# Performance work log

Measured on AMD Instinct MI355X. Metric: run time of the kernel, lower is better.

## Reference

```python
import jax, jax.numpy as jnp
import numpy as np

B = 16
C = 80
LEVELS = [(128, 128, 8), (64, 64, 16), (32, 32, 32), (16, 16, 64), (8, 8, 128)]
TOPN = 1000
MIN_SCORE = 0.05
NMS_THR = 0.6
MAX_OBJ = 100


def setup_inputs() -> dict:
    key = jax.random.key(0)
    inp = {}
    for l, (H, W, s) in enumerate(LEVELS):
        key, k1, k2, k3 = jax.random.split(key, 4)
        inp[f"cls{l}"] = jax.random.uniform(k1, (B, H, W, C), jnp.float32)
        inp[f"reg{l}"] = jax.random.uniform(k2, (B, H, W, 4), jnp.float32) * 128.0
        inp[f"ctr{l}"] = jax.random.uniform(k3, (B, H, W, 1), jnp.float32)
        xs = (jnp.arange(W, dtype=jnp.float32) + 0.5) * s
        ys = (jnp.arange(H, dtype=jnp.float32) + 0.5) * s
        gx, gy = jnp.meshgrid(xs, ys)  # [H, W]
        pos = jnp.stack([gx, gy], axis=-1)  # [H, W, 2]
        inp[f"pos{l}"] = jnp.broadcast_to(pos, (B, H, W, 2))
    return inp


def _nms_one(scores, classes, bboxes):
    # scores [N], classes int32 [N], bboxes float [N, 4] (already int-truncated values)
    s = jnp.where(scores > MIN_SCORE, scores, -jnp.inf)  # score-threshold mask
    top_s, top_i = jax.lax.top_k(s, TOPN)  # sort descending, keep topn
    top_c = jax.lax.stop_gradient(classes[top_i].astype(jnp.float32))
    top_b = bboxes[top_i]
    valid = top_s > MIN_SCORE
    wh = top_b[:, 2:4] - top_b[:, 0:2]
    areas = jnp.clip(wh[:, 0] * wh[:, 1], 0.0001)
    ar = jnp.arange(TOPN)

    def body(i, suppressed):
        active = valid[i] & (~suppressed[i])
        b = top_b[i]
        tl = jnp.maximum(b[0:2], top_b[:, 0:2])
        br = jnp.minimum(b[2:4], top_b[:, 2:4])
        owh = jnp.clip(br - tl, 0.0)
        inter = owh[:, 0] * owh[:, 1]
        union = jnp.clip(areas[i] + areas - inter, 0.0001)
        iou = inter / union
        return suppressed | (active & (ar > i) & (iou >= NMS_THR))

    suppressed = jax.lax.fori_loop(0, TOPN, body, jnp.zeros((TOPN,), bool))
    keep = valid & (~suppressed)
    rank = jnp.cumsum(keep.astype(jnp.int32)) - 1
    # scatter kept detections (in score order) into first MAX_OBJ slots; slot MAX_OBJ is a dump
    idx = jnp.where(keep & (rank < MAX_OBJ), rank, MAX_OBJ)
    out_s = jnp.full((MAX_OBJ + 1,), -1.0, jnp.float32).at[idx].set(jnp.where(keep, top_s, -1.0))[:MAX_OBJ]
    out_c = jnp.full((MAX_OBJ + 1,), -1.0, jnp.float32).at[idx].set(jnp.where(keep, top_c, -1.0))[:MAX_OBJ]
    out_b = jnp.zeros((MAX_OBJ + 1, 4), jnp.float32).at[idx].set(jnp.where(keep[:, None], top_b, 0.0))[:MAX_OBJ]
    return out_s, out_c, out_b


def _forward(cls_list, reg_list, ctr_list, pos_list):
    ss, cc, bb = [], [], []
    for c, r, t, p in zip(cls_list, reg_list, ctr_list, pos_list):
        b = c.shape[0]
        c = c.reshape(b, -1, c.shape[-1])   # [B, HW, 80]
        r = r.reshape(b, -1, 4)             # [B, HW, 4]
        t = t.reshape(b, -1)                # [B, HW]
        p = p.reshape(b, -1, 2)             # [B, HW, 2]
        sc = jnp.sqrt(jnp.max(c, axis=2) * t)
        cl = jnp.argmax(c, axis=2).astype(jnp.int32)
        bmin = p - r[:, :, 0:2]
        bmax = p + r[:, :, 2:4]
        # torch .int() truncates toward zero; values are used as floats afterward
        box = jax.lax.stop_gradient(jnp.trunc(jnp.concatenate([bmin, bmax], axis=2)))
        ss.append(sc); cc.append(cl); bb.append(box)
    scores = jnp.concatenate(ss, axis=1)
    classes = jnp.concatenate(cc, axis=1)
    boxes = jnp.concatenate(bb, axis=1)
    return jax.vmap(_nms_one)(scores, classes, boxes)


def reference(cls0, cls1, cls2, cls3, cls4, reg0, reg1, reg2, reg3, reg4,
              ctr0, ctr1, ctr2, ctr3, ctr4, pos0, pos1, pos2, pos3, pos4):
    return _forward([cls0, cls1, cls2, cls3, cls4],
                    [reg0, reg1, reg2, reg3, reg4],
                    [ctr0, ctr1, ctr2, ctr3, ctr4],
                    [pos0, pos1, pos2, pos3, pos4])
```

## Files before the change

### kernel.cpp

```cpp
#include <hip/hip_runtime.h>
#include <stdint.h>

typedef unsigned int u32;
typedef unsigned long long u64;

#define NTOT 21824
#define NBATCH 16
#define TOPN 1000
#define MAXOBJ 100
#define CAP 2048
#define CAPC 8192

__global__ void zero_kernel(u32* __restrict__ h) {
    int i = blockIdx.x * 1024 + threadIdx.x;
    if (i < NBATCH * 2048 + NBATCH * 32) h[i] = 0;
}

__global__ __launch_bounds__(256) void decode_kernel(
    const float* __restrict__ cls0, const float* __restrict__ cls1,
    const float* __restrict__ cls2, const float* __restrict__ cls3,
    const float* __restrict__ cls4,
    const float* __restrict__ ctr0, const float* __restrict__ ctr1,
    const float* __restrict__ ctr2, const float* __restrict__ ctr3,
    const float* __restrict__ ctr4,
    u32* __restrict__ keys, int* __restrict__ clsidx,
    u32* __restrict__ hist0)
{
    __shared__ u32 bh[2048];
    for (int i = threadIdx.x; i < 2048; i += 256) bh[i] = 0;
    __syncthreads();

    int tid = threadIdx.x;
    int g = tid >> 2, j = tid & 3;
    int loc = blockIdx.x * 64 + g;
    int b = blockIdx.y;
    if (loc < NTOT) {
        const float *cp, *tp;
        if (loc < 16384)      { size_t o = (size_t)b*16384 + loc;          cp = cls0 + o*80; tp = ctr0 + o; }
        else if (loc < 20480) { size_t o = (size_t)b*4096  + (loc-16384);  cp = cls1 + o*80; tp = ctr1 + o; }
        else if (loc < 21504) { size_t o = (size_t)b*1024  + (loc-20480);  cp = cls2 + o*80; tp = ctr2 + o; }
        else if (loc < 21760) { size_t o = (size_t)b*256   + (loc-21504);  cp = cls3 + o*80; tp = ctr3 + o; }
        else                  { size_t o = (size_t)b*64    + (loc-21760);  cp = cls4 + o*80; tp = ctr4 + o; }

        const float4* c4 = (const float4*)cp;
        float maxv = -1.0f; int arg = 0;
#pragma unroll
        for (int q = 0; q < 5; ++q) {
            float4 v = c4[j + 4*q];
            int ch = 16*q + 4*j;
            if (v.x > maxv) { maxv = v.x; arg = ch;     }
            if (v.y > maxv) { maxv = v.y; arg = ch + 1; }
            if (v.z > maxv) { maxv = v.z; arg = ch + 2; }
            if (v.w > maxv) { maxv = v.w; arg = ch + 3; }
        }
#pragma unroll
        for (int d = 1; d <= 2; d <<= 1) {
            float ov = __shfl_xor(maxv, d);
            int   oa = __shfl_xor(arg, d);
            if (ov > maxv || (ov == maxv && oa < arg)) { maxv = ov; arg = oa; }
        }
        if (j == 0) {
            float score = sqrtf(maxv * (*tp));
            u32 key = (score > 0.05f) ? (__float_as_uint(score) | 0x80000000u) : 0u;
            size_t o = (size_t)b * NTOT + loc;
            keys[o] = key;
            clsidx[o] = arg;
            if (key) atomicAdd(&bh[key >> 21], 1u);
        }
    }
    __syncthreads();
    for (int i = threadIdx.x; i < 2048; i += 256) {
        u32 c = bh[i];
        if (c) atomicAdd(&hist0[b * 2048 + i], c);
    }
}

__global__ __launch_bounds__(1024) void pivot_kernel(
    const u32* __restrict__ keys, const u32* __restrict__ hist0,
    u32* __restrict__ params,
    float* __restrict__ tscore, float* __restrict__ tcls, float4* __restrict__ tbox)
{
    __shared__ u32 shist[2048];
    __shared__ u32 s_wtot[16];
    __shared__ int s_tf;
    __shared__ u32 s_C, s_above;
    int b = blockIdx.x, tid = threadIdx.x;
    int lane = tid & 63, wave = tid >> 6;
    const u32* kb = keys + (size_t)b * NTOT;

    for (int i = tid; i < TOPN; i += 1024) {
        size_t o = (size_t)b * TOPN + i;
        tscore[o] = -1.0f; tcls[o] = -1.0f;
        tbox[o] = make_float4(0.f, 0.f, 0.f, 0.f);
    }

    u32 h0 = hist0[b * 2048 + 2 * tid];
    u32 h1 = hist0[b * 2048 + 2 * tid + 1];
    if (tid == 0) s_tf = -1;
    u32 x = h0 + h1;
#pragma unroll
    for (int off = 1; off < 64; off <<= 1) {
        u32 y = __shfl_down(x, off);
        if (lane + off < 64) x += y;
    }
    if (lane == 0) s_wtot[wave] = x;
    __syncthreads();
    u32 wsuf = 0, tot = 0;
    for (int w2 = 0; w2 < 16; ++w2) { u32 v = s_wtot[w2]; tot += v; if (w2 > wave) wsuf += v; }
    u32 suf0 = x + wsuf, suf1 = suf0 - h0;
    u32 target = (tot < TOPN) ? tot : TOPN;

    if (target > 0) {
        if (suf0 >= target) atomicMax(&s_tf, 2 * tid);
        if (suf1 >= target) atomicMax(&s_tf, 2 * tid + 1);
    }
    __syncthreads();
    int t0 = s_tf;
    if (target > 0) {
        if (2 * tid == t0)     { s_C = suf0; s_above = suf0 - h0; }
        if (2 * tid + 1 == t0) { s_C = suf1; s_above = suf1 - h1; }
    }
    __syncthreads();
    u32 C0 = (target > 0) ? s_C : 0;
    u32 above0 = (target > 0) ? s_above : 0;

    bool need2 = (target > 0 && C0 > CAP);
    int t1 = 0; u32 C1 = 0, above1 = 0;
    shist[2 * tid] = 0; shist[2 * tid + 1] = 0;
    if (tid == 0) s_tf = -1;
    __syncthreads();
    if (need2) {
        for (int i = tid; i < NTOT; i += 1024) {
            u32 k = kb[i];
            if (k && (int)(k >> 21) == t0) atomicAdd(&shist[(k >> 10) & 2047], 1u);
        }
    }
    __syncthreads();
    {
        u32 g0 = shist[2 * tid], g1 = shist[2 * tid + 1];
        u32 x2 = g0 + g1;
#pragma unroll
        for (int off = 1; off < 64; off <<= 1) {
            u32 y = __shfl_down(x2, off);
            if (lane + off < 64) x2 += y;
        }
        if (lane == 0) s_wtot[wave] = x2;
        __syncthreads();
        u32 ws2 = 0;
        for (int w2 = wave + 1; w2 < 16; ++w2) ws2 += s_wtot[w2];
        u32 sa0 = x2 + ws2, sa1 = sa0 - g0;
        u32 need2c = target - above0;
        if (need2) {
            if (sa0 >= need2c) atomicMax(&s_tf, 2 * tid);
            if (sa1 >= need2c) atomicMax(&s_tf, 2 * tid + 1);
        }
        __syncthreads();
        t1 = s_tf;
        if (need2) {
            if (2 * tid == t1)     { s_C = above0 + sa0; s_above = above0 + sa0 - g0; }
            if (2 * tid + 1 == t1) { s_C = above0 + sa1; s_above = above0 + sa1 - g1; }
        }
        __syncthreads();
        if (need2) { C1 = s_C; above1 = s_above; }
    }

    bool need3 = (need2 && C1 > CAP);
    int t2 = 0;
    __syncthreads();
    shist[2 * tid] = 0; shist[2 * tid + 1] = 0;
    if (tid == 0) s_tf = -1;
    __syncthreads();
    if (need3) {
        for (int i = tid; i < NTOT; i += 1024) {
            u32 k = kb[i];
            if (k && (int)(k >> 21) == t0 && (int)((k >> 10) & 2047) == t1)
                atomicAdd(&shist[k & 1023], 1u);
        }
    }
    __syncthreads();
    {
        u32 g = shist[tid];
        u32 x3 = g;
#pragma unroll
        for (int off = 1; off < 64; off <<= 1) {
            u32 y = __shfl_down(x3, off);
            if (lane + off < 64) x3 += y;
        }
        if (lane == 0) s_wtot[wave] = x3;
        __syncthreads();
        u32 ws3 = 0;
        for (int w2 = wave + 1; w2 < 16; ++w2) ws3 += s_wtot[w2];
        u32 sb = x3 + ws3;
        if (need3) {
            u32 need3c = target - above1;
            if (sb >= need3c && tid < 1024) atomicMax(&s_tf, tid);
        }
        __syncthreads();
        t2 = s_tf;
    }

    if (tid == 0) {
        u32 P;
        if (target == 0)      P = 0xFFFFFFFFu;
        else if (!need2)      P = (u32)t0 << 21;
        else if (!need3)      P = ((u32)t0 << 21) | ((u32)t1 << 10);
        else                  P = ((u32)t0 << 21) | ((u32)t1 << 10) | (u32)t2;
        params[2 * b] = P;
        params[2 * b + 1] = target;
    }
}

__global__ __launch_bounds__(256) void gather_kernel(
    const u32* __restrict__ keys, const u32* __restrict__ params,
    u64* __restrict__ candbuf, u32* __restrict__ gcnt)
{
    __shared__ u32 s_wcnt[4];
    __shared__ u32 s_base;
    int b = blockIdx.y;
    int tid = threadIdx.x;
    int lane = tid & 63, wave = tid >> 6;
    u32 P = params[2 * b];
    int i = blockIdx.x * 256 + tid;
    u32 k = (i < NTOT) ? keys[(size_t)b * NTOT + i] : 0u;
    bool pass = (k != 0u) && (k >= P);
    u64 mask = __ballot(pass);
    if (lane == 0) s_wcnt[wave] = (u32)__popcll(mask);
    __syncthreads();
    if (tid == 0) {
        u32 tot = s_wcnt[0] + s_wcnt[1] + s_wcnt[2] + s_wcnt[3];
        s_base = tot ? atomicAdd(&gcnt[b * 32], tot) : 0u;
    }
    __syncthreads();
    if (pass) {
        u32 woff = 0;
        for (int w2 = 0; w2 < wave; ++w2) woff += s_wcnt[w2];
        u32 pos = s_base + woff + (u32)__popcll(mask & ((1ull << lane) - 1ull));
        if (pos < CAPC)
            candbuf[(size_t)b * CAPC + pos] = ((u64)k << 32) | (u32)(~i);
    }
}

__global__ __launch_bounds__(256) void rank_kernel(
    const u64* __restrict__ candbuf, const u32* __restrict__ gcnt,
    const u32* __restrict__ params,
    const int* __restrict__ clsidx,
    const float* __restrict__ reg0, const float* __restrict__ reg1,
    const float* __restrict__ reg2, const float* __restrict__ reg3,
    const float* __restrict__ reg4,
    float* __restrict__ tscore, float* __restrict__ tcls, float4* __restrict__ tbox)
{
    int b = blockIdx.y;
    int lane = threadIdx.x & 63;
    u32 M = gcnt[b * 32]; if (M > CAPC) M = CAPC;
    u32 target = params[2 * b + 1];
    const u64* cb = candbuf + (size_t)b * CAPC;
    u32 Mr = (M + 63u) & ~63u;

    u32 wbase0 = blockIdx.x * 256 + (threadIdx.x & ~63u);
    for (u32 base = wbase0; base < M; base += 8 * 256) {
        u32 i0 = base + lane;
        bool val = (i0 < M);
        u64 e = val ? cb[i0] : ~0ull;
        u32 r = 0;
        for (u32 c0 = 0; c0 < Mr; c0 += 64) {
            u32 j = c0 + lane;
            u64 v = (j < M) ? cb[j] : 0ull;
            u32 vlo = (u32)v, vhi = (u32)(v >> 32);
#pragma unroll
            for (int s = 0; s < 64; ++s) {
                u32 lo = (u32)__builtin_amdgcn_readlane((int)vlo, s);
                u32 hi = (u32)__builtin_amdgcn_readlane((int)vhi, s);
                u64 vj = ((u64)hi << 32) | lo;
                r += (vj > e) ? 1u : 0u;
            }
        }
        if (val && r < target) {
            u32 k = (u32)(e >> 32);
            u32 loc = ~(u32)e;
            const float* rp; float st; u32 li; int wsh;
            if (loc < 16384u)      { li = loc;          wsh = 7; st = 8.f;   rp = reg0 + ((size_t)b*16384 + li)*4; }
            else if (loc < 20480u) { li = loc - 16384u; wsh = 6; st = 16.f;  rp = reg1 + ((size_t)b*4096  + li)*4; }
            else if (loc < 21504u) { li = loc - 20480u; wsh = 5; st = 32.f;  rp = reg2 + ((size_t)b*1024  + li)*4; }
            else if (loc < 21760u) { li = loc - 21504u; wsh = 4; st = 64.f;  rp = reg3 + ((size_t)b*256   + li)*4; }
            else                   { li = loc - 21760u; wsh = 3; st = 128.f; rp = reg4 + ((size_t)b*64    + li)*4; }
            u32 wx = li & ((1u << wsh) - 1u);
            u32 hy = li >> wsh;
            float px = ((float)wx + 0.5f) * st;
            float py = ((float)hy + 0.5f) * st;
            float4 rg = *(const float4*)rp;
            float4 bx;
            bx.x = truncf(px - rg.x); bx.y = truncf(py - rg.y);
            bx.z = truncf(px + rg.z); bx.w = truncf(py + rg.w);
            size_t src = (size_t)b * NTOT + loc;
            size_t o = (size_t)b * TOPN + r;
            tscore[o] = __uint_as_float(k & 0x7FFFFFFFu);
            tcls[o] = (float)clsidx[src];
            tbox[o] = bx;
        }
    }
}

__global__ __launch_bounds__(256) void iou_kernel(
    const float4* __restrict__ tbox, u64* __restrict__ sup)
{
    __shared__ float4 sbox[TOPN];
    int b = blockIdx.y;
    int tid = threadIdx.x, lane = tid & 63, wave = tid >> 6;
    const float4* tb = tbox + (size_t)b * TOPN;
    for (int i = tid; i < TOPN; i += 256) sbox[i] = tb[i];
    __syncthreads();
    int i = blockIdx.x * 4 + wave;
    float4 bi = sbox[i];
    float areai = fmaxf((bi.z - bi.x) * (bi.w - bi.y), 0.0001f);
    u64* row = sup + ((size_t)b * TOPN + i) * 16;
#pragma unroll
    for (int w = 0; w < 16; ++w) {
        int col = w * 64 + lane;
        bool bit = false;
        if (col < TOPN) {
            float4 bj = sbox[col];
            float areaj = fmaxf((bj.z - bj.x) * (bj.w - bj.y), 0.0001f);
            float tlx = fmaxf(bi.x, bj.x), tly = fmaxf(bi.y, bj.y);
            float brx = fminf(bi.z, bj.z), bry = fminf(bi.w, bj.w);
            float ow = fmaxf(brx - tlx, 0.f), oh = fmaxf(bry - tly, 0.f);
            float inter = ow * oh;
            float uni = fmaxf(areai + areaj - inter, 0.0001f);
            bit = (col > i) && (inter / uni >= 0.6f);
        }
        u64 m = __ballot(bit);
        if (lane == 0) row[w] = m;
    }
}

#define CHROWS 128
#define NCHUNK 8

__global__ __launch_bounds__(1024) void finalize_kernel(
    const float* __restrict__ tscore, const float* __restrict__ tcls,
    const float4* __restrict__ tbox, const u64* __restrict__ sup,
    float* __restrict__ out)
{
    __shared__ u64 mat[2][CHROWS * 16];
    __shared__ u32 validsh[TOPN];
    __shared__ u64 removed_sh[16];
    __shared__ u32 wpref[17];
    int b = blockIdx.x, tid = threadIdx.x;
    int wave = tid >> 6, lane = tid & 63;

    for (int i = tid; i < TOPN; i += 1024)
        validsh[i] = (tscore[(size_t)b * TOPN + i] > 0.05f) ? 1u : 0u;

    const u64* supb = sup + (size_t)b * TOPN * 16;
    for (int idx = tid; idx < CHROWS * 16; idx += 1024)
        mat[0][idx] = supb[idx];
    __syncthreads();

    u64 my = 0;
    if (wave == 0) {
#pragma unroll
        for (int w2 = 0; w2 < 16; ++w2) {
            int i = w2 * 64 + lane;
            bool v = (i < TOPN) ? (validsh[i] != 0) : false;
            u64 m = __ballot(v);
            if (lane == w2) my = ~m;
        }
    }

    for (int chunk = 0; chunk < NCHUNK; ++chunk) {
        if (wave > 0 && chunk + 1 < NCHUNK) {
            int nr = (chunk + 1 == NCHUNK - 1) ? (TOPN - (NCHUNK - 1) * CHROWS) : CHROWS;
            const u64* src = supb + (size_t)(chunk + 1) * CHROWS * 16;
            u64* dst = mat[(chunk + 1) & 1];
            for (int idx = tid - 64; idx < nr * 16; idx += 960)
                dst[idx] = src[idx];
        }
        if (wave == 0) {
            int r0 = chunk * CHROWS;
            int rows = (chunk == NCHUNK - 1) ? (TOPN - r0) : CHROWS;
            int lw = lane & 15;
            const u64* M = mat[chunk & 1];
            for (int sub = 0; sub < rows; sub += 64) {
                int w2 = (r0 + sub) >> 6;
                u64 cur = __shfl(my, w2);
                int nsub = rows - sub; if (nsub > 64) nsub = 64;
                const u64* R = M + sub * 16;
                int ngrp = nsub >> 3;
                u64 cme[8], cww[8];
#pragma unroll
                for (int g = 0; g < 8; ++g) { cme[g] = R[g*16 + lw]; cww[g] = R[g*16 + w2]; }
                for (int grp = 0; grp < ngrp; ++grp) {
                    u64 nme[8] = {0,0,0,0,0,0,0,0}, nww[8] = {0,0,0,0,0,0,0,0};
                    if (grp + 1 < ngrp) {
                        const u64* Rn = R + (grp + 1) * 128;
#pragma unroll
                        for (int g = 0; g < 8; ++g) { nme[g] = Rn[g*16 + lw]; nww[g] = Rn[g*16 + w2]; }
                    }
#pragma unroll
                    for (int g = 0; g < 8; ++g) {
                        int u = grp * 8 + g;
                        u64 bit = (cur >> u) & 1ull;
                        u64 act = bit - 1ull;
                        cur |= cww[g] & act;
                        my  |= cme[g] & act;
                    }
#pragma unroll
                    for (int g = 0; g < 8; ++g) { cme[g] = nme[g]; cww[g] = nww[g]; }
                }
            }
        }
        __syncthreads();
    }
    if (wave == 0) {
        if (lane < 16) removed_sh[lane] = my;
        u32 pc = (lane < 16) ? (u32)__popcll(~my) : 0u;
#pragma unroll
        for (int off = 1; off < 16; off <<= 1) {
            u32 y = __shfl_up(pc, off);
            if (lane >= off) pc += y;
        }
        if (lane < 16) wpref[lane + 1] = pc;
        if (lane == 0) wpref[0] = 0;
    }
    __syncthreads();

    float* out_s = out;
    float* out_c = out + NBATCH * MAXOBJ;
    float* out_b = out + 2 * NBATCH * MAXOBJ;
    if (tid < MAXOBJ)     { out_s[b * MAXOBJ + tid] = -1.f; out_c[b * MAXOBJ + tid] = -1.f; }
    if (tid < MAXOBJ * 4) out_b[b * MAXOBJ * 4 + tid] = 0.f;
    __syncthreads();
    if (tid < TOPN) {
        u64 kw = ~removed_sh[tid >> 6];
        if ((kw >> (tid & 63)) & 1ull) {
            int rank = (int)wpref[tid >> 6] + (int)__popcll(kw & ((1ull << (tid & 63)) - 1ull));
            if (rank < MAXOBJ) {
                size_t o = (size_t)b * TOPN + tid;
                out_s[b * MAXOBJ + rank] = tscore[o];
                out_c[b * MAXOBJ + rank] = tcls[o];
                ((float4*)out_b)[b * MAXOBJ + rank] = tbox[o];
            }
        }
    }
}

extern "C" void kernel_launch(void* const* d_in, const int* in_sizes, int n_in,
                              void* d_out, int out_size, void* d_ws, size_t ws_size,
                              hipStream_t stream) {
    (void)in_sizes; (void)n_in; (void)out_size; (void)ws_size;
    const float* cls[5]; const float* reg[5]; const float* ctr[5];
    for (int l = 0; l < 5; ++l) {
        cls[l] = (const float*)d_in[4 * l + 0];
        reg[l] = (const float*)d_in[4 * l + 1];
        ctr[l] = (const float*)d_in[4 * l + 2];
    }
    char* w = (char*)d_ws;
    u32*    keys   = (u32*)(w + 0);
    int*    clsidx = (int*)(w + 1396736);
    float*  tscore = (float*)(w + 8380416);
    float*  tcls   = (float*)(w + 8444416);
    float4* tbox   = (float4*)(w + 8508416);
    u64*    sup    = (u64*)(w + 8764416);
    u64*    candbuf= (u64*)(w + 8764416);
    u32*    hist0  = (u32*)(w + 9812992);
    u32*    gcnt   = (u32*)(w + 9944064);
    u32*    params = (u32*)(w + 9946112);

    zero_kernel<<<33, 1024, 0, stream>>>(hist0);
    decode_kernel<<<dim3((NTOT + 63) / 64, NBATCH), 256, 0, stream>>>(
        cls[0], cls[1], cls[2], cls[3], cls[4],
        ctr[0], ctr[1], ctr[2], ctr[3], ctr[4],
        keys, clsidx, hist0);
    pivot_kernel<<<NBATCH, 1024, 0, stream>>>(keys, hist0, params, tscore, tcls, tbox);
    gather_kernel<<<dim3((NTOT + 255) / 256, NBATCH), 256, 0, stream>>>(keys, params, candbuf, gcnt);
    rank_kernel<<<dim3(8, NBATCH), 256, 0, stream>>>(candbuf, gcnt, params, clsidx,
                                                     reg[0], reg[1], reg[2], reg[3], reg[4],
                                                     tscore, tcls, tbox);
    iou_kernel<<<dim3(TOPN / 4, NBATCH), 256, 0, stream>>>(tbox, sup);
    finalize_kernel<<<NBATCH, 1024, 0, stream>>>(tscore, tcls, tbox, sup, (float*)d_out);
}
```

Baseline: 277.1 us.

## Fuse histogram and candidate gather into pivot kernel, drop zero and gather launches

Moves the coarse key histogram out of decode and into the per-batch pivot block, which now builds it in shared memory by scanning its own keys. The candidate gather is folded into the same block using a shared counter, so the zero-init and gather kernels and their global atomics go away. This saves two launches and the global histogram traffic. In exchange, each batch's histogram and gather now run on a single 1024-thread block, which rescans all 21824 keys twice with far less parallelism.

```diff
diff --git a/kernel.cpp b/kernel.cpp
--- a/kernel.cpp
+++ b/kernel.cpp
@@ -10,11 +10,6 @@
 #define MAXOBJ 100
 #define CAP 2048
 #define CAPC 8192
-
-__global__ void zero_kernel(u32* __restrict__ h) {
-    int i = blockIdx.x * 1024 + threadIdx.x;
-    if (i < NBATCH * 2048 + NBATCH * 32) h[i] = 0;
-}
 
 __global__ __launch_bounds__(256) void decode_kernel(
     const float* __restrict__ cls0, const float* __restrict__ cls1,
@@ -23,67 +18,56 @@
     const float* __restrict__ ctr0, const float* __restrict__ ctr1,
     const float* __restrict__ ctr2, const float* __restrict__ ctr3,
     const float* __restrict__ ctr4,
-    u32* __restrict__ keys, int* __restrict__ clsidx,
-    u32* __restrict__ hist0)
+    u32* __restrict__ keys, int* __restrict__ clsidx)
 {
-    __shared__ u32 bh[2048];
-    for (int i = threadIdx.x; i < 2048; i += 256) bh[i] = 0;
-    __syncthreads();
-
     int tid = threadIdx.x;
     int g = tid >> 2, j = tid & 3;
     int loc = blockIdx.x * 64 + g;
     int b = blockIdx.y;
-    if (loc < NTOT) {
-        const float *cp, *tp;
-        if (loc < 16384)      { size_t o = (size_t)b*16384 + loc;          cp = cls0 + o*80; tp = ctr0 + o; }
-        else if (loc < 20480) { size_t o = (size_t)b*4096  + (loc-16384);  cp = cls1 + o*80; tp = ctr1 + o; }
-        else if (loc < 21504) { size_t o = (size_t)b*1024  + (loc-20480);  cp = cls2 + o*80; tp = ctr2 + o; }
-        else if (loc < 21760) { size_t o = (size_t)b*256   + (loc-21504);  cp = cls3 + o*80; tp = ctr3 + o; }
-        else                  { size_t o = (size_t)b*64    + (loc-21760);  cp = cls4 + o*80; tp = ctr4 + o; }
-
-        const float4* c4 = (const float4*)cp;
-        float maxv = -1.0f; int arg = 0;
-#pragma unroll
-        for (int q = 0; q < 5; ++q) {
-            float4 v = c4[j + 4*q];
-            int ch = 16*q + 4*j;
-            if (v.x > maxv) { maxv = v.x; arg = ch;     }
-            if (v.y > maxv) { maxv = v.y; arg = ch + 1; }
-            if (v.z > maxv) { maxv = v.z; arg = ch + 2; }
-            if (v.w > maxv) { maxv = v.w; arg = ch + 3; }
-        }
-#pragma unroll
-        for (int d = 1; d <= 2; d <<= 1) {
-            float ov = __shfl_xor(maxv, d);
-            int   oa = __shfl_xor(arg, d);
-            if (ov > maxv || (ov == maxv && oa < arg)) { maxv = ov; arg = oa; }
-        }
-        if (j == 0) {
-            float score = sqrtf(maxv * (*tp));
-            u32 key = (score > 0.05f) ? (__float_as_uint(score) | 0x80000000u) : 0u;
-            size_t o = (size_t)b * NTOT + loc;
-            keys[o] = key;
-            clsidx[o] = arg;
-            if (key) atomicAdd(&bh[key >> 21], 1u);
-        }
-    }
-    __syncthreads();
-    for (int i = threadIdx.x; i < 2048; i += 256) {
-        u32 c = bh[i];
-        if (c) atomicAdd(&hist0[b * 2048 + i], c);
+    if (loc >= NTOT) return;
+
+    const float *cp, *tp;
+    if (loc < 16384)      { size_t o = (size_t)b*16384 + loc;          cp = cls0 + o*80; tp = ctr0 + o; }
+    else if (loc < 20480) { size_t o = (size_t)b*4096  + (loc-16384);  cp = cls1 + o*80; tp = ctr1 + o; }
+    else if (loc < 21504) { size_t o = (size_t)b*1024  + (loc-20480);  cp = cls2 + o*80; tp = ctr2 + o; }
+    else if (loc < 21760) { size_t o = (size_t)b*256   + (loc-21504);  cp = cls3 + o*80; tp = ctr3 + o; }
+    else                  { size_t o = (size_t)b*64    + (loc-21760);  cp = cls4 + o*80; tp = ctr4 + o; }
+
+    const float4* c4 = (const float4*)cp;
+    float maxv = -1.0f; int arg = 0;
+#pragma unroll
+    for (int q = 0; q < 5; ++q) {
+        float4 v = c4[j + 4*q];
+        int ch = 16*q + 4*j;
+        if (v.x > maxv) { maxv = v.x; arg = ch;     }
+        if (v.y > maxv) { maxv = v.y; arg = ch + 1; }
+        if (v.z > maxv) { maxv = v.z; arg = ch + 2; }
+        if (v.w > maxv) { maxv = v.w; arg = ch + 3; }
+    }
+#pragma unroll
+    for (int d = 1; d <= 2; d <<= 1) {
+        float ov = __shfl_xor(maxv, d);
+        int   oa = __shfl_xor(arg, d);
+        if (ov > maxv || (ov == maxv && oa < arg)) { maxv = ov; arg = oa; }
+    }
+    if (j == 0) {
+        float score = sqrtf(maxv * (*tp));
+        u32 key = (score > 0.05f) ? (__float_as_uint(score) | 0x80000000u) : 0u;
+        size_t o = (size_t)b * NTOT + loc;
+        keys[o] = key;
+        clsidx[o] = arg;
     }
 }
 
 __global__ __launch_bounds__(1024) void pivot_kernel(
-    const u32* __restrict__ keys, const u32* __restrict__ hist0,
-    u32* __restrict__ params,
+    const u32* __restrict__ keys,
+    u64* __restrict__ candbuf, u32* __restrict__ params,
     float* __restrict__ tscore, float* __restrict__ tcls, float4* __restrict__ tbox)
 {
     __shared__ u32 shist[2048];
     __shared__ u32 s_wtot[16];
     __shared__ int s_tf;
-    __shared__ u32 s_C, s_above;
+    __shared__ u32 s_C, s_above, s_P, s_cnt;
     int b = blockIdx.x, tid = threadIdx.x;
     int lane = tid & 63, wave = tid >> 6;
     const u32* kb = keys + (size_t)b * NTOT;
@@ -94,8 +78,16 @@
         tbox[o] = make_float4(0.f, 0.f, 0.f, 0.f);
     }
 
-    u32 h0 = hist0[b * 2048 + 2 * tid];
-    u32 h1 = hist0[b * 2048 + 2 * tid + 1];
+    shist[2 * tid] = 0; shist[2 * tid + 1] = 0;
+    __syncthreads();
+    for (int i = tid; i < NTOT; i += 1024) {
+        u32 k = kb[i];
+        if (k) atomicAdd(&shist[k >> 21], 1u);
+    }
+    __syncthreads();
+
+    u32 h0 = shist[2 * tid];
+    u32 h1 = shist[2 * tid + 1];
     if (tid == 0) s_tf = -1;
     u32 x = h0 + h1;
 #pragma unroll
@@ -205,44 +197,36 @@
         else if (!need2)      P = (u32)t0 << 21;
         else if (!need3)      P = ((u32)t0 << 21) | ((u32)t1 << 10);
         else                  P = ((u32)t0 << 21) | ((u32)t1 << 10) | (u32)t2;
-        params[2 * b] = P;
-        params[2 * b + 1] = target;
-    }
-}
-
-__global__ __launch_bounds__(256) void gather_kernel(
-    const u32* __restrict__ keys, const u32* __restrict__ params,
-    u64* __restrict__ candbuf, u32* __restrict__ gcnt)
-{
-    __shared__ u32 s_wcnt[4];
-    __shared__ u32 s_base;
-    int b = blockIdx.y;
-    int tid = threadIdx.x;
-    int lane = tid & 63, wave = tid >> 6;
-    u32 P = params[2 * b];
-    int i = blockIdx.x * 256 + tid;
-    u32 k = (i < NTOT) ? keys[(size_t)b * NTOT + i] : 0u;
-    bool pass = (k != 0u) && (k >= P);
-    u64 mask = __ballot(pass);
-    if (lane == 0) s_wcnt[wave] = (u32)__popcll(mask);
+        s_P = P;
+        s_cnt = 0;
+        params[4 * b] = target;
+    }
+    __syncthreads();
+
+    u32 P = s_P;
+    for (int base = 0; base < NTOT; base += 1024) {
+        int i = base + tid;
+        u32 k = (i < NTOT) ? kb[i] : 0u;
+        bool pass = (k != 0u) && (k >= P);
+        u64 mask = __ballot(pass);
+        u32 wbase = 0;
+        if (lane == 0 && mask) wbase = atomicAdd(&s_cnt, (u32)__popcll(mask));
+        wbase = __shfl(wbase, 0);
+        if (pass) {
+            u32 pos = wbase + (u32)__popcll(mask & ((1ull << lane) - 1ull));
+            if (pos < CAPC)
+                candbuf[(size_t)b * CAPC + pos] = ((u64)k << 32) | (u32)(~i);
+        }
+    }
     __syncthreads();
     if (tid == 0) {
-        u32 tot = s_wcnt[0] + s_wcnt[1] + s_wcnt[2] + s_wcnt[3];
-        s_base = tot ? atomicAdd(&gcnt[b * 32], tot) : 0u;
-    }
-    __syncthreads();
-    if (pass) {
-        u32 woff = 0;
-        for (int w2 = 0; w2 < wave; ++w2) woff += s_wcnt[w2];
-        u32 pos = s_base + woff + (u32)__popcll(mask & ((1ull << lane) - 1ull));
-        if (pos < CAPC)
-            candbuf[(size_t)b * CAPC + pos] = ((u64)k << 32) | (u32)(~i);
+        u32 M = s_cnt; if (M > CAPC) M = CAPC;
+        params[4 * b + 1] = M;
     }
 }
 
 __global__ __launch_bounds__(256) void rank_kernel(
-    const u64* __restrict__ candbuf, const u32* __restrict__ gcnt,
-    const u32* __restrict__ params,
+    const u64* __restrict__ candbuf, const u32* __restrict__ params,
     const int* __restrict__ clsidx,
     const float* __restrict__ reg0, const float* __restrict__ reg1,
     const float* __restrict__ reg2, const float* __restrict__ reg3,
@@ -251,8 +235,8 @@
 {
     int b = blockIdx.y;
     int lane = threadIdx.x & 63;
-    u32 M = gcnt[b * 32]; if (M > CAPC) M = CAPC;
-    u32 target = params[2 * b + 1];
+    u32 target = params[4 * b];
+    u32 M = params[4 * b + 1];
     const u64* cb = candbuf + (size_t)b * CAPC;
     u32 Mr = (M + 63u) & ~63u;
 
@@ -456,23 +440,19 @@
     char* w = (char*)d_ws;
     u32*    keys   = (u32*)(w + 0);
     int*    clsidx = (int*)(w + 1396736);
-    float*  tscore = (float*)(w + 8380416);
-    float*  tcls   = (float*)(w + 8444416);
-    float4* tbox   = (float4*)(w + 8508416);
-    u64*    sup    = (u64*)(w + 8764416);
-    u64*    candbuf= (u64*)(w + 8764416);
-    u32*    hist0  = (u32*)(w + 9812992);
-    u32*    gcnt   = (u32*)(w + 9944064);
-    u32*    params = (u32*)(w + 9946112);
-
-    zero_kernel<<<33, 1024, 0, stream>>>(hist0);
+    float*  tscore = (float*)(w + 2793472);
+    float*  tcls   = (float*)(w + 2857472);
+    float4* tbox   = (float4*)(w + 2921472);
+    u64*    sup    = (u64*)(w + 3177472);
+    u64*    candbuf= (u64*)(w + 3177472);
+    u32*    params = (u32*)(w + 5225472);
+
     decode_kernel<<<dim3((NTOT + 63) / 64, NBATCH), 256, 0, stream>>>(
         cls[0], cls[1], cls[2], cls[3], cls[4],
         ctr[0], ctr[1], ctr[2], ctr[3], ctr[4],
-        keys, clsidx, hist0);
-    pivot_kernel<<<NBATCH, 1024, 0, stream>>>(keys, hist0, params, tscore, tcls, tbox);
-    gather_kernel<<<dim3((NTOT + 255) / 256, NBATCH), 256, 0, stream>>>(keys, params, candbuf, gcnt);
-    rank_kernel<<<dim3(8, NBATCH), 256, 0, stream>>>(candbuf, gcnt, params, clsidx,
+        keys, clsidx);
+    pivot_kernel<<<NBATCH, 1024, 0, stream>>>(keys, candbuf, params, tscore, tcls, tbox);
+    rank_kernel<<<dim3(8, NBATCH), 256, 0, stream>>>(candbuf, params, clsidx,
                                                      reg[0], reg[1], reg[2], reg[3], reg[4],
                                                      tscore, tcls, tbox);
     iou_kernel<<<dim3(TOPN / 4, NBATCH), 256, 0, stream>>>(tbox, sup);
```

Result: no change. 282.1 us (+1.8%).

## Replace multi-pass radix top-k pivot with a single 32K-bin global histogram

Applied to the files above, without the earlier changes.

The decode kernel now atomically adds each valid key straight into a per-batch 32768-bin global histogram indexed by the upper 16 bits of the score key. This replaces the block-shared 2048-bin histogram. The pivot kernel finds the threshold bin with one suffix scan over that histogram, so it no longer rescans all keys for second- and third-level refinement passes. In exchange it zeroes a 2 MB histogram on every call and issues many more global atomics from decode. The pivot bin may also hold more candidates than before, which puts more load on the candidate buffer and the rank stage.

```diff
diff --git a/kernel.cpp b/kernel.cpp
--- a/kernel.cpp
+++ b/kernel.cpp
@@ -8,12 +8,12 @@
 #define NBATCH 16
 #define TOPN 1000
 #define MAXOBJ 100
-#define CAP 2048
 #define CAPC 8192
-
-__global__ void zero_kernel(u32* __restrict__ h) {
+#define NBINS 32768
+
+__global__ __launch_bounds__(1024) void zero_kernel(u32* __restrict__ h) {
     int i = blockIdx.x * 1024 + threadIdx.x;
-    if (i < NBATCH * 2048 + NBATCH * 32) h[i] = 0;
+    if (i < NBATCH * NBINS + NBATCH * 32) h[i] = 0;
 }
 
 __global__ __launch_bounds__(256) void decode_kernel(
@@ -23,81 +23,71 @@
     const float* __restrict__ ctr0, const float* __restrict__ ctr1,
     const float* __restrict__ ctr2, const float* __restrict__ ctr3,
     const float* __restrict__ ctr4,
-    u32* __restrict__ keys, int* __restrict__ clsidx,
-    u32* __restrict__ hist0)
-{
-    __shared__ u32 bh[2048];
-    for (int i = threadIdx.x; i < 2048; i += 256) bh[i] = 0;
-    __syncthreads();
-
+    u32* __restrict__ keys, int* __restrict__ clsidx, u32* __restrict__ hist)
+{
     int tid = threadIdx.x;
     int g = tid >> 2, j = tid & 3;
     int loc = blockIdx.x * 64 + g;
     int b = blockIdx.y;
-    if (loc < NTOT) {
-        const float *cp, *tp;
-        if (loc < 16384)      { size_t o = (size_t)b*16384 + loc;          cp = cls0 + o*80; tp = ctr0 + o; }
-        else if (loc < 20480) { size_t o = (size_t)b*4096  + (loc-16384);  cp = cls1 + o*80; tp = ctr1 + o; }
-        else if (loc < 21504) { size_t o = (size_t)b*1024  + (loc-20480);  cp = cls2 + o*80; tp = ctr2 + o; }
-        else if (loc < 21760) { size_t o = (size_t)b*256   + (loc-21504);  cp = cls3 + o*80; tp = ctr3 + o; }
-        else                  { size_t o = (size_t)b*64    + (loc-21760);  cp = cls4 + o*80; tp = ctr4 + o; }
-
-        const float4* c4 = (const float4*)cp;
-        float maxv = -1.0f; int arg = 0;
-#pragma unroll
-        for (int q = 0; q < 5; ++q) {
-            float4 v = c4[j + 4*q];
-            int ch = 16*q + 4*j;
-            if (v.x > maxv) { maxv = v.x; arg = ch;     }
-            if (v.y > maxv) { maxv = v.y; arg = ch + 1; }
-            if (v.z > maxv) { maxv = v.z; arg = ch + 2; }
-            if (v.w > maxv) { maxv = v.w; arg = ch + 3; }
-        }
-#pragma unroll
-        for (int d = 1; d <= 2; d <<= 1) {
-            float ov = __shfl_xor(maxv, d);
-            int   oa = __shfl_xor(arg, d);
-            if (ov > maxv || (ov == maxv && oa < arg)) { maxv = ov; arg = oa; }
-        }
-        if (j == 0) {
-            float score = sqrtf(maxv * (*tp));
-            u32 key = (score > 0.05f) ? (__float_as_uint(score) | 0x80000000u) : 0u;
-            size_t o = (size_t)b * NTOT + loc;
-            keys[o] = key;
-            clsidx[o] = arg;
-            if (key) atomicAdd(&bh[key >> 21], 1u);
-        }
-    }
-    __syncthreads();
-    for (int i = threadIdx.x; i < 2048; i += 256) {
-        u32 c = bh[i];
-        if (c) atomicAdd(&hist0[b * 2048 + i], c);
+    if (loc >= NTOT) return;
+
+    const float *cp, *tp;
+    if (loc < 16384)      { size_t o = (size_t)b*16384 + loc;          cp = cls0 + o*80; tp = ctr0 + o; }
+    else if (loc < 20480) { size_t o = (size_t)b*4096  + (loc-16384);  cp = cls1 + o*80; tp = ctr1 + o; }
+    else if (loc < 21504) { size_t o = (size_t)b*1024  + (loc-20480);  cp = cls2 + o*80; tp = ctr2 + o; }
+    else if (loc < 21760) { size_t o = (size_t)b*256   + (loc-21504);  cp = cls3 + o*80; tp = ctr3 + o; }
+    else                  { size_t o = (size_t)b*64    + (loc-21760);  cp = cls4 + o*80; tp = ctr4 + o; }
+
+    const float4* c4 = (const float4*)cp;
+    float maxv = -1.0f; int arg = 0;
+#pragma unroll
+    for (int q = 0; q < 5; ++q) {
+        float4 v = c4[j + 4*q];
+        int ch = 16*q + 4*j;
+        if (v.x > maxv) { maxv = v.x; arg = ch;     }
+        if (v.y > maxv) { maxv = v.y; arg = ch + 1; }
+        if (v.z > maxv) { maxv = v.z; arg = ch + 2; }
+        if (v.w > maxv) { maxv = v.w; arg = ch + 3; }
+    }
+#pragma unroll
+    for (int d = 1; d <= 2; d <<= 1) {
+        float ov = __shfl_xor(maxv, d);
+        int   oa = __shfl_xor(arg, d);
+        if (ov > maxv || (ov == maxv && oa < arg)) { maxv = ov; arg = oa; }
+    }
+    if (j == 0) {
+        float score = sqrtf(maxv * (*tp));
+        u32 key = (score > 0.05f) ? (__float_as_uint(score) | 0x80000000u) : 0u;
+        size_t o = (size_t)b * NTOT + loc;
+        keys[o] = key;
+        clsidx[o] = arg;
+        if (key) atomicAdd(&hist[b * NBINS + ((key >> 16) & (NBINS - 1))], 1u);
     }
 }
 
 __global__ __launch_bounds__(1024) void pivot_kernel(
-    const u32* __restrict__ keys, const u32* __restrict__ hist0,
-    u32* __restrict__ params,
+    const u32* __restrict__ hist, u32* __restrict__ params,
     float* __restrict__ tscore, float* __restrict__ tcls, float4* __restrict__ tbox)
 {
-    __shared__ u32 shist[2048];
     __shared__ u32 s_wtot[16];
     __shared__ int s_tf;
-    __shared__ u32 s_C, s_above;
     int b = blockIdx.x, tid = threadIdx.x;
     int lane = tid & 63, wave = tid >> 6;
-    const u32* kb = keys + (size_t)b * NTOT;
+    const u32* hb = hist + (size_t)b * NBINS;
+    int base = tid * 32;
 
     for (int i = tid; i < TOPN; i += 1024) {
         size_t o = (size_t)b * TOPN + i;
         tscore[o] = -1.0f; tcls[o] = -1.0f;
         tbox[o] = make_float4(0.f, 0.f, 0.f, 0.f);
     }
-
-    u32 h0 = hist0[b * 2048 + 2 * tid];
-    u32 h1 = hist0[b * 2048 + 2 * tid + 1];
     if (tid == 0) s_tf = -1;
-    u32 x = h0 + h1;
+
+    u32 s = 0;
+#pragma unroll 8
+    for (int j = 0; j < 32; ++j) s += hb[base + j];
+
+    u32 x = s;
 #pragma unroll
     for (int off = 1; off < 64; off <<= 1) {
         u32 y = __shfl_down(x, off);
@@ -107,104 +97,24 @@
     __syncthreads();
     u32 wsuf = 0, tot = 0;
     for (int w2 = 0; w2 < 16; ++w2) { u32 v = s_wtot[w2]; tot += v; if (w2 > wave) wsuf += v; }
-    u32 suf0 = x + wsuf, suf1 = suf0 - h0;
+    u32 suffix_incl = x + wsuf;
+    u32 suffix_above = suffix_incl - s;
     u32 target = (tot < TOPN) ? tot : TOPN;
 
-    if (target > 0) {
-        if (suf0 >= target) atomicMax(&s_tf, 2 * tid);
-        if (suf1 >= target) atomicMax(&s_tf, 2 * tid + 1);
-    }
-    __syncthreads();
-    int t0 = s_tf;
-    if (target > 0) {
-        if (2 * tid == t0)     { s_C = suf0; s_above = suf0 - h0; }
-        if (2 * tid + 1 == t0) { s_C = suf1; s_above = suf1 - h1; }
-    }
-    __syncthreads();
-    u32 C0 = (target > 0) ? s_C : 0;
-    u32 above0 = (target > 0) ? s_above : 0;
-
-    bool need2 = (target > 0 && C0 > CAP);
-    int t1 = 0; u32 C1 = 0, above1 = 0;
-    shist[2 * tid] = 0; shist[2 * tid + 1] = 0;
-    if (tid == 0) s_tf = -1;
-    __syncthreads();
-    if (need2) {
-        for (int i = tid; i < NTOT; i += 1024) {
-            u32 k = kb[i];
-            if (k && (int)(k >> 21) == t0) atomicAdd(&shist[(k >> 10) & 2047], 1u);
-        }
-    }
-    __syncthreads();
-    {
-        u32 g0 = shist[2 * tid], g1 = shist[2 * tid + 1];
-        u32 x2 = g0 + g1;
-#pragma unroll
-        for (int off = 1; off < 64; off <<= 1) {
-            u32 y = __shfl_down(x2, off);
-            if (lane + off < 64) x2 += y;
-        }
-        if (lane == 0) s_wtot[wave] = x2;
-        __syncthreads();
-        u32 ws2 = 0;
-        for (int w2 = wave + 1; w2 < 16; ++w2) ws2 += s_wtot[w2];
-        u32 sa0 = x2 + ws2, sa1 = sa0 - g0;
-        u32 need2c = target - above0;
-        if (need2) {
-            if (sa0 >= need2c) atomicMax(&s_tf, 2 * tid);
-            if (sa1 >= need2c) atomicMax(&s_tf, 2 * tid + 1);
-        }
-        __syncthreads();
-        t1 = s_tf;
-        if (need2) {
-            if (2 * tid == t1)     { s_C = above0 + sa0; s_above = above0 + sa0 - g0; }
-            if (2 * tid + 1 == t1) { s_C = above0 + sa1; s_above = above0 + sa1 - g1; }
-        }
-        __syncthreads();
-        if (need2) { C1 = s_C; above1 = s_above; }
-    }
-
-    bool need3 = (need2 && C1 > CAP);
-    int t2 = 0;
-    __syncthreads();
-    shist[2 * tid] = 0; shist[2 * tid + 1] = 0;
-    if (tid == 0) s_tf = -1;
-    __syncthreads();
-    if (need3) {
-        for (int i = tid; i < NTOT; i += 1024) {
-            u32 k = kb[i];
-            if (k && (int)(k >> 21) == t0 && (int)((k >> 10) & 2047) == t1)
-                atomicAdd(&shist[k & 1023], 1u);
-        }
-    }
-    __syncthreads();
-    {
-        u32 g = shist[tid];
-        u32 x3 = g;
-#pragma unroll
-        for (int off = 1; off < 64; off <<= 1) {
-            u32 y = __shfl_down(x3, off);
-            if (lane + off < 64) x3 += y;
-        }
-        if (lane == 0) s_wtot[wave] = x3;
-        __syncthreads();
-        u32 ws3 = 0;
-        for (int w2 = wave + 1; w2 < 16; ++w2) ws3 += s_wtot[w2];
-        u32 sb = x3 + ws3;
-        if (need3) {
-            u32 need3c = target - above1;
-            if (sb >= need3c && tid < 1024) atomicMax(&s_tf, tid);
-        }
-        __syncthreads();
-        t2 = s_tf;
-    }
-
+    if (target > 0 && suffix_incl >= target) {
+        u32 run = suffix_above;
+        for (int j = 31; j >= 0; --j) {
+            run += hb[base + j];
+            if (run >= target) { atomicMax(&s_tf, base + j); break; }
+        }
+    }
+    __syncthreads();
     if (tid == 0) {
+        int t0 = s_tf;
         u32 P;
-        if (target == 0)      P = 0xFFFFFFFFu;
-        else if (!need2)      P = (u32)t0 << 21;
-        else if (!need3)      P = ((u32)t0 << 21) | ((u32)t1 << 10);
-        else                  P = ((u32)t0 << 21) | ((u32)t1 << 10) | (u32)t2;
+        if (target == 0)        P = 0xFFFFFFFFu;
+        else if (tot <= TOPN)   P = 1u;
+        else                    P = ((u32)t0 << 16) | 0x80000000u;
         params[2 * b] = P;
         params[2 * b + 1] = target;
     }
@@ -456,21 +366,21 @@
     char* w = (char*)d_ws;
     u32*    keys   = (u32*)(w + 0);
     int*    clsidx = (int*)(w + 1396736);
-    float*  tscore = (float*)(w + 8380416);
-    float*  tcls   = (float*)(w + 8444416);
-    float4* tbox   = (float4*)(w + 8508416);
-    u64*    sup    = (u64*)(w + 8764416);
-    u64*    candbuf= (u64*)(w + 8764416);
-    u32*    hist0  = (u32*)(w + 9812992);
-    u32*    gcnt   = (u32*)(w + 9944064);
-    u32*    params = (u32*)(w + 9946112);
-
-    zero_kernel<<<33, 1024, 0, stream>>>(hist0);
+    float*  tscore = (float*)(w + 2793472);
+    float*  tcls   = (float*)(w + 2857472);
+    float4* tbox   = (float4*)(w + 2921472);
+    u64*    sup    = (u64*)(w + 3177472);
+    u64*    candbuf= (u64*)(w + 3177472);
+    u32*    hist   = (u32*)(w + 5225472);
+    u32*    gcnt   = (u32*)(w + 7322624);
+    u32*    params = (u32*)(w + 7324672);
+
+    zero_kernel<<<(NBATCH * NBINS + NBATCH * 32 + 1023) / 1024, 1024, 0, stream>>>(hist);
     decode_kernel<<<dim3((NTOT + 63) / 64, NBATCH), 256, 0, stream>>>(
         cls[0], cls[1], cls[2], cls[3], cls[4],
         ctr[0], ctr[1], ctr[2], ctr[3], ctr[4],
-        keys, clsidx, hist0);
-    pivot_kernel<<<NBATCH, 1024, 0, stream>>>(keys, hist0, params, tscore, tcls, tbox);
+        keys, clsidx, hist);
+    pivot_kernel<<<NBATCH, 1024, 0, stream>>>(hist, params, tscore, tcls, tbox);
     gather_kernel<<<dim3((NTOT + 255) / 256, NBATCH), 256, 0, stream>>>(keys, params, candbuf, gcnt);
     rank_kernel<<<dim3(8, NBATCH), 256, 0, stream>>>(candbuf, gcnt, params, clsidx,
                                                      reg[0], reg[1], reg[2], reg[3], reg[4],
```

New measurement: 295.9 us. 6.8% more time.
